# Kernel tuning notes

Measured on AMD Instinct MI355X. Metric: run time of the kernel, lower is better.

Reference implementation:

```python
import jax, jax.numpy as jnp
import numpy as np

N_NODES = 100000
N_EDGES = 1600000
DIM_IN = 128
DIM_OUT = 128


def setup_inputs() -> dict:
    key = jax.random.key(0)
    k1, k2, k3 = jax.random.split(key, 3)
    x = jax.random.normal(k1, (N_NODES, DIM_IN), dtype=jnp.float32)
    W = jax.random.normal(k2, (DIM_OUT, DIM_IN), dtype=jnp.float32) * (1.0 / np.sqrt(DIM_IN))
    bias = jnp.zeros((DIM_OUT,), dtype=jnp.float32)
    edge_index = jax.random.randint(k3, (2, N_EDGES), 0, N_NODES, dtype=jnp.int64)
    return {"x": x, "W": W, "bias": bias, "edge_index": edge_index}


def reference(x, W, bias, edge_index):
    N = x.shape[0]
    # add self loops
    loops = jnp.arange(N, dtype=edge_index.dtype)
    row = jnp.concatenate([edge_index[0], loops])  # source nodes (x_j)
    col = jnp.concatenate([edge_index[1], loops])  # target nodes (aggregation)
    # linear transform (no bias inside lin)
    h = x @ W.T  # [N, out]
    # symmetric degree normalization, degree computed over col incl. self loops
    deg = jax.ops.segment_sum(jnp.ones_like(col, dtype=x.dtype), col, num_segments=N)
    deg_inv_sqrt = jnp.where(deg > 0, deg ** -0.5, 0.0)
    norm = deg_inv_sqrt[row] * deg_inv_sqrt[col]  # [E+N]
    # gather-scale-scatter_add
    msg = norm[:, None] * h[row]  # [E+N, out]
    out = jax.ops.segment_sum(msg, col, num_segments=N)
    return out + bias
```

## Files before the change

kernel.cpp:

```cpp
#include <hip/hip_runtime.h>

#define DIM 128
#define CAP 64
#define BUCKET_BLOCKS 1024
#define GEMM_BLOCKS 1568
#define GRID_COMBO (BUCKET_BLOCKS + GEMM_BLOCKS)


typedef __attribute__((ext_vector_type(8))) short bf16x8;
typedef __attribute__((ext_vector_type(4))) float f32x4;

__device__ __forceinline__ unsigned short f2bf(float f) {
  unsigned int u = __float_as_uint(f);
  return (unsigned short)((u + 0x7FFFu + ((u >> 16) & 1u)) >> 16);
}
__device__ __forceinline__ float bf2f(unsigned int s) {
  return __uint_as_float(s << 16);
}

__global__ __launch_bounds__(256) void prep_kernel(
    const float* __restrict__ W, unsigned short* __restrict__ Wb,
    int* __restrict__ cnt, int N) {
  int i = blockIdx.x * 256 + threadIdx.x;
  if (i < DIM * DIM) Wb[i] = f2bf(W[i]);
  if (i < N) cnt[i] = 0;
}

__global__ __launch_bounds__(256) void combo_kernel(
    const int* __restrict__ rows, const int* __restrict__ cols,
    int* __restrict__ cnt, int* __restrict__ csr,
    const float* __restrict__ x, const unsigned short* __restrict__ Wb,
    unsigned short* __restrict__ h, int E, int N) {
  if (blockIdx.x < BUCKET_BLOCKS) {
    int bid = blockIdx.x;
    int g = bid & 7;
    int gblk = bid >> 3;
    int lo = (int)((long long)g * N / 8);
    int hi = (int)((long long)(g + 1) * N / 8);
    const int4* cols4 = (const int4*)cols;
    int E4 = E >> 2;
    for (int i = gblk * 256 + threadIdx.x; i < E4;
         i += (BUCKET_BLOCKS / 8) * 256) {
      int4 c4 = cols4[i];
      int e = i * 4;
      if (c4.x >= lo && c4.x < hi) {
        int k = atomicAdd(&cnt[c4.x], 1);
        if (k < CAP) csr[(size_t)c4.x * CAP + k] = rows[e];
      }
      if (c4.y >= lo && c4.y < hi) {
        int k = atomicAdd(&cnt[c4.y], 1);
        if (k < CAP) csr[(size_t)c4.y * CAP + k] = rows[e + 1];
      }
      if (c4.z >= lo && c4.z < hi) {
        int k = atomicAdd(&cnt[c4.z], 1);
        if (k < CAP) csr[(size_t)c4.z * CAP + k] = rows[e + 2];
      }
      if (c4.w >= lo && c4.w < hi) {
        int k = atomicAdd(&cnt[c4.w], 1);
        if (k < CAP) csr[(size_t)c4.w * CAP + k] = rows[e + 3];
      }
    }
    if (gblk == 0) {
      for (int e = (E & ~3) + threadIdx.x; e < E; e += 256) {
        int c = cols[e];
        if (c >= lo && c < hi) {
          int k = atomicAdd(&cnt[c], 1);
          if (k < CAP) csr[(size_t)c * CAP + k] = rows[e];
        }
      }
    }
  } else {
    int wid = (blockIdx.x - BUCKET_BLOCKS) * 4 + (threadIdx.x >> 6);
    int m0 = wid * 16;
    if (m0 >= N) return;
    int lane = threadIdx.x & 63;
    int mr = lane & 15;
    int quad = lane >> 4;

    bf16x8 afrag[4];
    const float* xrow = x + (size_t)(m0 + mr) * DIM + quad * 8;
#pragma unroll
    for (int ks = 0; ks < 4; ++ks) {
      float4 lo = *(const float4*)(xrow + ks * 32);
      float4 hi = *(const float4*)(xrow + ks * 32 + 4);
      bf16x8 a;
      a[0] = (short)f2bf(lo.x); a[1] = (short)f2bf(lo.y);
      a[2] = (short)f2bf(lo.z); a[3] = (short)f2bf(lo.w);
      a[4] = (short)f2bf(hi.x); a[5] = (short)f2bf(hi.y);
      a[6] = (short)f2bf(hi.z); a[7] = (short)f2bf(hi.w);
      afrag[ks] = a;
    }

#pragma unroll
    for (int nt = 0; nt < 8; ++nt) {
      f32x4 c = {0.f, 0.f, 0.f, 0.f};
#pragma unroll
      for (int ks = 0; ks < 4; ++ks) {
        bf16x8 b = *(const bf16x8*)(Wb + (size_t)(nt * 16 + mr) * DIM +
                                    ks * 32 + quad * 8);
        c = __builtin_amdgcn_mfma_f32_16x16x32_bf16(afrag[ks], b, c, 0, 0, 0);
      }
#pragma unroll
      for (int r = 0; r < 4; ++r) {
        h[(size_t)(m0 + quad * 4 + r) * DIM + nt * 16 + mr] = f2bf(c[r]);
      }
    }
  }
}

__global__ __launch_bounds__(256) void gather_kernel(
    const uint4* __restrict__ h4, const int* __restrict__ csr,
    const int* __restrict__ cnt, const float4* __restrict__ bias4,
    float4* __restrict__ out4, int N) {
  int node = blockIdx.x * 16 + (threadIdx.x >> 4);
  if (node >= N) return;
  int lane = threadIdx.x & 15;

  int degN = cnt[node];
  float dn = rsqrtf((float)degN + 1.0f);
  int deg = degN > CAP ? CAP : degN;
  const int* seg = csr + (size_t)node * CAP;

  float acc[8];
  {
    uint4 s = h4[(size_t)node * 16 + lane];
    acc[0] = dn * bf2f(s.x & 0xFFFF); acc[1] = dn * bf2f(s.x >> 16);
    acc[2] = dn * bf2f(s.y & 0xFFFF); acc[3] = dn * bf2f(s.y >> 16);
    acc[4] = dn * bf2f(s.z & 0xFFFF); acc[5] = dn * bf2f(s.z >> 16);
    acc[6] = dn * bf2f(s.w & 0xFFFF); acc[7] = dn * bf2f(s.w >> 16);
  }
  for (int j = 0; j < deg; ++j) {
    int r = seg[j];
    float dr = rsqrtf((float)cnt[r] + 1.0f);
    uint4 v = h4[(size_t)r * 16 + lane];
    acc[0] += dr * bf2f(v.x & 0xFFFF); acc[1] += dr * bf2f(v.x >> 16);
    acc[2] += dr * bf2f(v.y & 0xFFFF); acc[3] += dr * bf2f(v.y >> 16);
    acc[4] += dr * bf2f(v.z & 0xFFFF); acc[5] += dr * bf2f(v.z >> 16);
    acc[6] += dr * bf2f(v.w & 0xFFFF); acc[7] += dr * bf2f(v.w >> 16);
  }
  float4 bA = bias4[lane * 2], bB = bias4[lane * 2 + 1];
  float4 oA = {dn * acc[0] + bA.x, dn * acc[1] + bA.y,
               dn * acc[2] + bA.z, dn * acc[3] + bA.w};
  float4 oB = {dn * acc[4] + bB.x, dn * acc[5] + bB.y,
               dn * acc[6] + bB.z, dn * acc[7] + bB.w};
  out4[(size_t)node * 32 + lane * 2]     = oA;
  out4[(size_t)node * 32 + lane * 2 + 1] = oB;
}

extern "C" void kernel_launch(void* const* d_in, const int* in_sizes, int n_in,
                              void* d_out, int out_size, void* d_ws, size_t ws_size,
                              hipStream_t stream) {
  const float* x    = (const float*)d_in[0];
  const float* W    = (const float*)d_in[1];
  const float* bias = (const float*)d_in[2];
  const int*   ei   = (const int*)d_in[3];

  const int N = in_sizes[0] / DIM;
  const int E = in_sizes[3] / 2;
  const int* rows = ei;
  const int* cols = ei + E;
  float* out = (float*)d_out;
  char* ws = (char*)d_ws;

  int* cnt = (int*)ws;
  unsigned short* Wb = (unsigned short*)(ws + 409600);
  int* csr = (int*)(ws + 442368);
  unsigned short* h = (unsigned short*)(ws + 26042368);

  prep_kernel<<<(N + 255) / 256, 256, 0, stream>>>(W, Wb, cnt, N);
  combo_kernel<<<GRID_COMBO, 256, 0, stream>>>(rows, cols, cnt, csr, x, Wb, h,
                                               E, N);
  gather_kernel<<<(N + 15) / 16, 256, 0, stream>>>(
      (const uint4*)h, csr, cnt, (const float4*)bias, (float4*)out, N);
}
```

Before: 274.4 us.

## Partition gather into source-slice passes with multi-node slots and nontemporal accesses

The gather kernel now assigns seven destination nodes to each 16-lane slot. It sweeps the neighbor lists eight times, each pass accepting only sources in one slice of the node range, with a per-block rotation. The aim is a smaller concurrently-touched slice of h so that neighbor feature reads hit cache more often. The cost is rereading each adjacency list eight times and holding many accumulators per thread. The bucketing pass skips loading row indices when no column in a vector matches, and the GEMM and output use nontemporal loads and stores.

After: 902.5 us. 3.29x slower.

```diff
diff --git a/kernel.cpp b/kernel.cpp
--- a/kernel.cpp
+++ b/kernel.cpp
@@ -6,9 +6,14 @@
 #define GEMM_BLOCKS 1568
 #define GRID_COMBO (BUCKET_BLOCKS + GEMM_BLOCKS)
 
+#define GATHER_BLOCKS 893
+#define SLOT_NODES 7
+#define NPASS 8
+
 
 typedef __attribute__((ext_vector_type(8))) short bf16x8;
 typedef __attribute__((ext_vector_type(4))) float f32x4;
+typedef __attribute__((ext_vector_type(4))) int i32x4;
 
 __device__ __forceinline__ unsigned short f2bf(float f) {
   unsigned int u = __float_as_uint(f);
@@ -16,6 +21,12 @@
 }
 __device__ __forceinline__ float bf2f(unsigned int s) {
   return __uint_as_float(s << 16);
+}
+__device__ __forceinline__ void acc8(float* a, uint4 v, float s) {
+  a[0] += s * bf2f(v.x & 0xFFFF); a[1] += s * bf2f(v.x >> 16);
+  a[2] += s * bf2f(v.y & 0xFFFF); a[3] += s * bf2f(v.y >> 16);
+  a[4] += s * bf2f(v.z & 0xFFFF); a[5] += s * bf2f(v.z >> 16);
+  a[6] += s * bf2f(v.w & 0xFFFF); a[7] += s * bf2f(v.w >> 16);
 }
 
 __global__ __launch_bounds__(256) void prep_kernel(
@@ -37,27 +48,34 @@
     int gblk = bid >> 3;
     int lo = (int)((long long)g * N / 8);
     int hi = (int)((long long)(g + 1) * N / 8);
-    const int4* cols4 = (const int4*)cols;
+    const i32x4* cols4 = (const i32x4*)cols;
+    const i32x4* rows4 = (const i32x4*)rows;
     int E4 = E >> 2;
     for (int i = gblk * 256 + threadIdx.x; i < E4;
          i += (BUCKET_BLOCKS / 8) * 256) {
-      int4 c4 = cols4[i];
-      int e = i * 4;
-      if (c4.x >= lo && c4.x < hi) {
-        int k = atomicAdd(&cnt[c4.x], 1);
-        if (k < CAP) csr[(size_t)c4.x * CAP + k] = rows[e];
-      }
-      if (c4.y >= lo && c4.y < hi) {
-        int k = atomicAdd(&cnt[c4.y], 1);
-        if (k < CAP) csr[(size_t)c4.y * CAP + k] = rows[e + 1];
-      }
-      if (c4.z >= lo && c4.z < hi) {
-        int k = atomicAdd(&cnt[c4.z], 1);
-        if (k < CAP) csr[(size_t)c4.z * CAP + k] = rows[e + 2];
-      }
-      if (c4.w >= lo && c4.w < hi) {
-        int k = atomicAdd(&cnt[c4.w], 1);
-        if (k < CAP) csr[(size_t)c4.w * CAP + k] = rows[e + 3];
+      i32x4 c4 = cols4[i];
+      bool mx = (c4.x >= lo) & (c4.x < hi);
+      bool my = (c4.y >= lo) & (c4.y < hi);
+      bool mz = (c4.z >= lo) & (c4.z < hi);
+      bool mw = (c4.w >= lo) & (c4.w < hi);
+      if (mx | my | mz | mw) {
+        i32x4 r4 = rows4[i];
+        if (mx) {
+          int k = atomicAdd(&cnt[c4.x], 1);
+          if (k < CAP) csr[(size_t)c4.x * CAP + k] = r4.x;
+        }
+        if (my) {
+          int k = atomicAdd(&cnt[c4.y], 1);
+          if (k < CAP) csr[(size_t)c4.y * CAP + k] = r4.y;
+        }
+        if (mz) {
+          int k = atomicAdd(&cnt[c4.z], 1);
+          if (k < CAP) csr[(size_t)c4.z * CAP + k] = r4.z;
+        }
+        if (mw) {
+          int k = atomicAdd(&cnt[c4.w], 1);
+          if (k < CAP) csr[(size_t)c4.w * CAP + k] = r4.w;
+        }
       }
     }
     if (gblk == 0) {
@@ -81,8 +99,8 @@
     const float* xrow = x + (size_t)(m0 + mr) * DIM + quad * 8;
 #pragma unroll
     for (int ks = 0; ks < 4; ++ks) {
-      float4 lo = *(const float4*)(xrow + ks * 32);
-      float4 hi = *(const float4*)(xrow + ks * 32 + 4);
+      f32x4 lo = __builtin_nontemporal_load((const f32x4*)(xrow + ks * 32));
+      f32x4 hi = __builtin_nontemporal_load((const f32x4*)(xrow + ks * 32 + 4));
       bf16x8 a;
       a[0] = (short)f2bf(lo.x); a[1] = (short)f2bf(lo.y);
       a[2] = (short)f2bf(lo.z); a[3] = (short)f2bf(lo.w);
@@ -102,49 +120,73 @@
       }
 #pragma unroll
       for (int r = 0; r < 4; ++r) {
-        h[(size_t)(m0 + quad * 4 + r) * DIM + nt * 16 + mr] = f2bf(c[r]);
-      }
-    }
-  }
-}
-
-__global__ __launch_bounds__(256) void gather_kernel(
+        unsigned short hv = f2bf(c[r]);
+        __builtin_nontemporal_store(
+            hv, &h[(size_t)(m0 + quad * 4 + r) * DIM + nt * 16 + mr]);
+      }
+    }
+  }
+}
+
+__global__ __launch_bounds__(256, 4) void gather_kernel(
     const uint4* __restrict__ h4, const int* __restrict__ csr,
     const int* __restrict__ cnt, const float4* __restrict__ bias4,
-    float4* __restrict__ out4, int N) {
-  int node = blockIdx.x * 16 + (threadIdx.x >> 4);
-  if (node >= N) return;
+    float* __restrict__ out, int N) {
+  int slot = threadIdx.x >> 4;
   int lane = threadIdx.x & 15;
-
-  int degN = cnt[node];
-  float dn = rsqrtf((float)degN + 1.0f);
-  int deg = degN > CAP ? CAP : degN;
-  const int* seg = csr + (size_t)node * CAP;
-
-  float acc[8];
-  {
-    uint4 s = h4[(size_t)node * 16 + lane];
-    acc[0] = dn * bf2f(s.x & 0xFFFF); acc[1] = dn * bf2f(s.x >> 16);
-    acc[2] = dn * bf2f(s.y & 0xFFFF); acc[3] = dn * bf2f(s.y >> 16);
-    acc[4] = dn * bf2f(s.z & 0xFFFF); acc[5] = dn * bf2f(s.z >> 16);
-    acc[6] = dn * bf2f(s.w & 0xFFFF); acc[7] = dn * bf2f(s.w >> 16);
-  }
-  for (int j = 0; j < deg; ++j) {
-    int r = seg[j];
-    float dr = rsqrtf((float)cnt[r] + 1.0f);
-    uint4 v = h4[(size_t)r * 16 + lane];
-    acc[0] += dr * bf2f(v.x & 0xFFFF); acc[1] += dr * bf2f(v.x >> 16);
-    acc[2] += dr * bf2f(v.y & 0xFFFF); acc[3] += dr * bf2f(v.y >> 16);
-    acc[4] += dr * bf2f(v.z & 0xFFFF); acc[5] += dr * bf2f(v.z >> 16);
-    acc[6] += dr * bf2f(v.w & 0xFFFF); acc[7] += dr * bf2f(v.w >> 16);
-  }
+  int base = (blockIdx.x * 16 + slot) * SLOT_NODES;
+  int grp = blockIdx.x & 7;
+
+  float acc[SLOT_NODES][8];
+#pragma unroll
+  for (int n = 0; n < SLOT_NODES; ++n) {
+    int node = base + n;
+#pragma unroll
+    for (int i = 0; i < 8; ++i) acc[n][i] = 0.f;
+    if (node < N) {
+      float dn = rsqrtf((float)cnt[node] + 1.0f);
+      uint4 v = h4[(size_t)node * 16 + lane];
+      acc8(acc[n], v, dn);
+    }
+  }
+
+  for (int p = 0; p < NPASS; ++p) {
+    int slice = (p + grp) & (NPASS - 1);
+    int lo = (int)((long long)slice * N / NPASS);
+    int hi = (int)((long long)(slice + 1) * N / NPASS);
+#pragma unroll
+    for (int n = 0; n < SLOT_NODES; ++n) {
+      int node = base + n;
+      if (node >= N) continue;
+      int degN = cnt[node];
+      int deg = degN > CAP ? CAP : degN;
+      const int* seg = csr + (size_t)node * CAP;
+      for (int j = 0; j < deg; ++j) {
+        int r = __builtin_nontemporal_load(seg + j);
+        if (r >= lo && r < hi) {
+          float dr = rsqrtf((float)cnt[r] + 1.0f);
+          uint4 v = h4[(size_t)r * 16 + lane];
+          acc8(acc[n], v, dr);
+        }
+      }
+    }
+  }
+
   float4 bA = bias4[lane * 2], bB = bias4[lane * 2 + 1];
-  float4 oA = {dn * acc[0] + bA.x, dn * acc[1] + bA.y,
-               dn * acc[2] + bA.z, dn * acc[3] + bA.w};
-  float4 oB = {dn * acc[4] + bB.x, dn * acc[5] + bB.y,
-               dn * acc[6] + bB.z, dn * acc[7] + bB.w};
-  out4[(size_t)node * 32 + lane * 2]     = oA;
-  out4[(size_t)node * 32 + lane * 2 + 1] = oB;
+  f32x4* outv = (f32x4*)out;
+#pragma unroll
+  for (int n = 0; n < SLOT_NODES; ++n) {
+    int node = base + n;
+    if (node >= N) continue;
+    float dn = rsqrtf((float)cnt[node] + 1.0f);
+    f32x4 oA = {dn * acc[n][0] + bA.x, dn * acc[n][1] + bA.y,
+                dn * acc[n][2] + bA.z, dn * acc[n][3] + bA.w};
+    f32x4 oB = {dn * acc[n][4] + bB.x, dn * acc[n][5] + bB.y,
+                dn * acc[n][6] + bB.z, dn * acc[n][7] + bB.w};
+    size_t o = (size_t)node * 32 + lane * 2;
+    __builtin_nontemporal_store(oA, &outv[o]);
+    __builtin_nontemporal_store(oB, &outv[o + 1]);
+  }
 }
 
 extern "C" void kernel_launch(void* const* d_in, const int* in_sizes, int n_in,
@@ -170,6 +212,6 @@
   prep_kernel<<<(N + 255) / 256, 256, 0, stream>>>(W, Wb, cnt, N);
   combo_kernel<<<GRID_COMBO, 256, 0, stream>>>(rows, cols, cnt, csr, x, Wb, h,
                                                E, N);
-  gather_kernel<<<(N + 15) / 16, 256, 0, stream>>>(
-      (const uint4*)h, csr, cnt, (const float4*)bias, (float4*)out, N);
-}
+  gather_kernel<<<GATHER_BLOCKS, 256, 0, stream>>>(
+      (const uint4*)h, csr, cnt, (const float4*)bias, out, N);
+}
```
